# Optimization experiments

Measured on AMD Instinct MI355X. Metric: run time of the kernel, lower is better.

Reference implementation:

```python
import jax, jax.numpy as jnp
import numpy as np

B, S, K, N = 4, 2048, 4096, 4096

def setup_inputs() -> dict:
    key = jax.random.key(0)
    k1, k2, k3, k4 = jax.random.split(key, 4)
    # int8 quantized activations and weight (stored as int8, matmul accumulates int32)
    a = jax.random.randint(k1, (B, S, K), -128, 128, dtype=jnp.int32).astype(jnp.int8)
    w = jax.random.randint(k3, (K, N), -128, 128, dtype=jnp.int32).astype(jnp.int8)
    # dequant scales: per-token for activations, per-output-channel for weight
    a_s = (jax.random.uniform(k2, (B, S, 1), dtype=jnp.float32) + 0.5) * 0.01
    w_s = (jax.random.uniform(k4, (1, N), dtype=jnp.float32) + 0.5) * 0.01
    return {"a": a, "a_s": a_s, "w": w, "w_s": w_s}

def reference(a, a_s, w, w_s):
    # torch._int_mm loop with padding), fused with dequant epilogue.
    acc = jnp.einsum('bsk,kn->bsn', a, w, preferred_element_type=jnp.int32)
    # dequant: float32 accum * input_scale * weight_scale, cast to model dtype (fp16)
    out = (acc.astype(jnp.float32) * a_s * w_s).astype(jnp.float16)
    return out
```

## Files before the change

kernel.cpp:

```cpp
#include <hip/hip_runtime.h>
#include <cstdint>
#include <cstddef>


#define M_DIM 8192
#define N_DIM 4096
#define K_DIM 4096

#define PACKA_BLOCKS ((M_DIM * K_DIM / 4) / 256)
#define TRANS_BLOCKS ((N_DIM / 64) * (K_DIM / 64))

typedef int v4i  __attribute__((ext_vector_type(4)));
typedef int v16i __attribute__((ext_vector_type(16)));

__device__ __forceinline__ uint32_t pack4(int x, int y, int z, int w)
{
    return (uint32_t)(x & 0xff) | ((uint32_t)(y & 0xff) << 8) |
           ((uint32_t)(z & 0xff) << 16) | ((uint32_t)(w & 0xff) << 24);
}

__global__ void __launch_bounds__(256) prepare_kernel(
    const int* __restrict__ a, const int* __restrict__ w,
    uint8_t* __restrict__ pa, uint8_t* __restrict__ wt)
{
    __shared__ int lds[64][65];

    if (blockIdx.x < PACKA_BLOCKS) {
        const size_t idx = (size_t)blockIdx.x * 256 + threadIdx.x;
        int4 x = ((const int4*)a)[idx];
        ((uint32_t*)pa)[idx] = pack4(x.x, x.y, x.z, x.w);
        return;
    }

    const int tile = blockIdx.x - PACKA_BLOCKS;
    const int t  = threadIdx.x;
    const int n0 = (tile & 63) * 64;
    const int k0 = (tile >> 6) * 64;

#pragma unroll
    for (int i = 0; i < 4; ++i) {
        int v   = t + 256 * i;
        int row = v >> 4;
        int cq  = v & 15;
        int4 x = *(const int4*)(w + (size_t)(k0 + row) * N_DIM + n0 + cq * 4);
        lds[row][cq * 4 + 0] = x.x;
        lds[row][cq * 4 + 1] = x.y;
        lds[row][cq * 4 + 2] = x.z;
        lds[row][cq * 4 + 3] = x.w;
    }
    __syncthreads();

    const int n_local = t >> 2;
    const int c       = t & 3;
    uint32_t o[4];
#pragma unroll
    for (int j = 0; j < 4; ++j)
        o[j] = pack4(lds[c * 16 + j * 4 + 0][n_local],
                     lds[c * 16 + j * 4 + 1][n_local],
                     lds[c * 16 + j * 4 + 2][n_local],
                     lds[c * 16 + j * 4 + 3][n_local]);
    *(uint4*)(wt + (size_t)(n0 + n_local) * K_DIM + k0 + c * 16) =
        make_uint4(o[0], o[1], o[2], o[3]);
}

__device__ __forceinline__ void async_copy16(const void* gptr, void* lptr)
{
    __builtin_amdgcn_global_load_lds(
        (const __attribute__((address_space(1))) uint32_t*)gptr,
        (__attribute__((address_space(3))) uint32_t*)lptr,
        16, 0, 0);
}

#define VMCNT0() asm volatile("s_waitcnt vmcnt(0)" ::: "memory")

__global__ void __launch_bounds__(512, 2) int8_gemm_kernel(
    const uint8_t* __restrict__ A,
    const uint8_t* __restrict__ Wt,
    const float*   __restrict__ a_s,
    const float*   __restrict__ w_s,
    float*         __restrict__ out)
{
    __shared__ __align__(16) uint8_t sA[2][4][8][1024];
    __shared__ __align__(16) uint8_t sB[2][4][8][1024];

    const int tid   = threadIdx.x;
    const int wave  = tid >> 6;
    const int lane  = tid & 63;
    const int waveM = wave >> 2;
    const int waveN = wave & 3;

    const int bid = blockIdx.x;
    const int xc  = bid & 7;
    const int j   = bid >> 3;
    const int bm  = (xc & 3) * 8 + (j & 7);
    const int bn  = (xc >> 2) * 8 + (j >> 3);
    const int m0  = bm * 256;
    const int n0  = bn * 256;

    v16i acc[4][2];
#pragma unroll
    for (int i = 0; i < 4; ++i)
#pragma unroll
        for (int jj = 0; jj < 2; ++jj)
#pragma unroll
            for (int r = 0; r < 16; ++r)
                acc[i][jj][r] = 0;

    const uint8_t* aSrc = A  + (size_t)(m0 + wave * 32 + (lane & 31)) * K_DIM
                             + ((lane >> 5) << 4);
    const uint8_t* bSrc = Wt + (size_t)(n0 + wave * 32 + (lane & 31)) * K_DIM
                             + ((lane >> 5) << 4);

    auto stage_tile = [&](int buf, int kt) {
        const int ko = kt * 128;
#pragma unroll
        for (int s = 0; s < 4; ++s) {
            async_copy16(aSrc + ko + s * 32, &sA[buf][s][wave][0]);
            async_copy16(bSrc + ko + s * 32, &sB[buf][s][wave][0]);
        }
    };

    auto compute_kstep = [&](int buf, int s) {
        v4i af[4], bf[2];
#pragma unroll
        for (int mt = 0; mt < 4; ++mt)
            af[mt] = *(const v4i*)(&sA[buf][s][waveM * 4 + mt][lane * 16]);
#pragma unroll
        for (int nt = 0; nt < 2; ++nt)
            bf[nt] = *(const v4i*)(&sB[buf][s][waveN * 2 + nt][lane * 16]);
        __builtin_amdgcn_s_setprio(1);
#pragma unroll
        for (int mt = 0; mt < 4; ++mt)
#pragma unroll
            for (int nt = 0; nt < 2; ++nt)
                acc[mt][nt] = __builtin_amdgcn_mfma_i32_32x32x32_i8(
                    af[mt], bf[nt], acc[mt][nt], 0, 0, 0);
        __builtin_amdgcn_s_setprio(0);
    };

    const int NT = K_DIM / 128;

    stage_tile(0, 0);
    VMCNT0();
    __builtin_amdgcn_s_barrier();

    for (int kt = 0; kt < NT - 1; ++kt) {
        const int b = kt & 1;
        stage_tile(b ^ 1, kt + 1);
#pragma unroll
        for (int s = 0; s < 4; ++s)
            compute_kstep(b, s);
        VMCNT0();
        __builtin_amdgcn_s_barrier();
    }
#pragma unroll
    for (int s = 0; s < 4; ++s)
        compute_kstep((NT - 1) & 1, s);

    const int col   = lane & 31;
    const int rbase = (lane >> 5) * 4;

#pragma unroll
    for (int mt = 0; mt < 4; ++mt) {
        const int mrow0 = m0 + waveM * 128 + mt * 32 + rbase;
        float asv[16];
#pragma unroll
        for (int reg = 0; reg < 16; ++reg)
            asv[reg] = a_s[mrow0 + (reg & 3) + 8 * (reg >> 2)];
#pragma unroll
        for (int nt = 0; nt < 2; ++nt) {
            const int n = n0 + waveN * 64 + nt * 32 + col;
            const float wsv = w_s[n];
#pragma unroll
            for (int reg = 0; reg < 16; ++reg) {
                const int row = mrow0 + (reg & 3) + 8 * (reg >> 2);
                float v = (float)acc[mt][nt][reg] * asv[reg] * wsv;
                v = (float)(_Float16)v;
                out[(size_t)row * N_DIM + n] = v;
            }
        }
    }
}

extern "C" void kernel_launch(void* const* d_in, const int* in_sizes, int n_in,
                              void* d_out, int out_size, void* d_ws, size_t ws_size,
                              hipStream_t stream)
{
    const int*   a   = (const int*)  d_in[0];
    const float* a_s = (const float*)d_in[1];
    const int*   w   = (const int*)  d_in[2];
    const float* w_s = (const float*)d_in[3];
    float*       out = (float*)d_out;

    uint8_t* wt = (uint8_t*)d_ws;
    uint8_t* pa = (uint8_t*)d_ws + (size_t)N_DIM * K_DIM;

    prepare_kernel<<<PACKA_BLOCKS + TRANS_BLOCKS, 256, 0, stream>>>(a, w, pa, wt);

    int8_gemm_kernel<<<(M_DIM / 256) * (N_DIM / 256), 512, 0, stream>>>(
        pa, wt, a_s, w_s, out);
}
```

Before: 460.5 us.

## Pre-swizzle A and W into MFMA fragment layout and split-phase pipeline loads

```diff
diff --git a/kernel.cpp b/kernel.cpp
--- a/kernel.cpp
+++ b/kernel.cpp
@@ -7,8 +7,8 @@
 #define N_DIM 4096
 #define K_DIM 4096
 
-#define PACKA_BLOCKS ((M_DIM * K_DIM / 4) / 256)
-#define TRANS_BLOCKS ((N_DIM / 64) * (K_DIM / 64))
+#define PREP_A_BLOCKS ((M_DIM / 32) * (K_DIM / 128))
+#define PREP_W_BLOCKS ((N_DIM / 64) * (K_DIM / 64))
 
 typedef int v4i  __attribute__((ext_vector_type(4)));
 typedef int v16i __attribute__((ext_vector_type(16)));
@@ -21,19 +21,36 @@
 
 __global__ void __launch_bounds__(256) prepare_kernel(
     const int* __restrict__ a, const int* __restrict__ w,
-    uint8_t* __restrict__ pa, uint8_t* __restrict__ wt)
+    uint8_t* __restrict__ a_f, uint8_t* __restrict__ w_f)
 {
     __shared__ int lds[64][65];
-
-    if (blockIdx.x < PACKA_BLOCKS) {
-        const size_t idx = (size_t)blockIdx.x * 256 + threadIdx.x;
-        int4 x = ((const int4*)a)[idx];
-        ((uint32_t*)pa)[idx] = pack4(x.x, x.y, x.z, x.w);
+    const int t = threadIdx.x;
+
+    if (blockIdx.x < PREP_A_BLOCKS) {
+        uint32_t* l32 = (uint32_t*)&lds[0][0];
+        const int bm = blockIdx.x >> 5;
+        const int bk = blockIdx.x & 31;
+        const int m0 = bm * 32;
+        const int k0 = bk * 128;
+#pragma unroll
+        for (int i = 0; i < 4; ++i) {
+            const int f = i * 256 + t;
+            const int r = f >> 5;
+            const int c = (f << 2) & 127;
+            int4 x = *(const int4*)(a + (size_t)(m0 + r) * K_DIM + k0 + c);
+            uint32_t u = pack4(x.x, x.y, x.z, x.w);
+            const int region = c >> 5;
+            const int chunk  = r + (((c >> 4) & 1) << 5);
+            const int wd     = region * 256 + chunk * 4 + ((c & 15) >> 2);
+            l32[wd ^ ((region & 3) << 3)] = u;
+        }
+        __syncthreads();
+        uint4 o = ((const uint4*)l32)[t ^ (((t >> 6) & 3) << 1)];
+        *(uint4*)(a_f + ((size_t)bm * 128 + bk * 4) * 1024 + t * 16) = o;
         return;
     }
 
-    const int tile = blockIdx.x - PACKA_BLOCKS;
-    const int t  = threadIdx.x;
+    const int tile = blockIdx.x - PREP_A_BLOCKS;
     const int n0 = (tile & 63) * 64;
     const int k0 = (tile >> 6) * 64;
 
@@ -50,17 +67,22 @@
     }
     __syncthreads();
 
-    const int n_local = t >> 2;
-    const int c       = t & 3;
+    const int chunk  = t & 63;
+    const int r_out  = t >> 6;
+    const int nb     = r_out >> 1;
+    const int kk     = r_out & 1;
+    const int ncol   = nb * 32 + (chunk & 31);
+    const int parity = chunk >> 5;
+    const int rbase  = kk * 32 + parity * 16;
     uint32_t o[4];
 #pragma unroll
-    for (int j = 0; j < 4; ++j)
-        o[j] = pack4(lds[c * 16 + j * 4 + 0][n_local],
-                     lds[c * 16 + j * 4 + 1][n_local],
-                     lds[c * 16 + j * 4 + 2][n_local],
-                     lds[c * 16 + j * 4 + 3][n_local]);
-    *(uint4*)(wt + (size_t)(n0 + n_local) * K_DIM + k0 + c * 16) =
-        make_uint4(o[0], o[1], o[2], o[3]);
+    for (int q = 0; q < 4; ++q)
+        o[q] = pack4(lds[rbase + q * 4 + 0][ncol],
+                     lds[rbase + q * 4 + 1][ncol],
+                     lds[rbase + q * 4 + 2][ncol],
+                     lds[rbase + q * 4 + 3][ncol]);
+    *(uint4*)(w_f + (((size_t)(n0 >> 5) + nb) * 128 + (k0 >> 5) + kk) * 1024
+                  + chunk * 16) = make_uint4(o[0], o[1], o[2], o[3]);
 }
 
 __device__ __forceinline__ void async_copy16(const void* gptr, void* lptr)
@@ -71,11 +93,12 @@
         16, 0, 0);
 }
 
+#define VMCNT4() asm volatile("s_waitcnt vmcnt(4)" ::: "memory")
 #define VMCNT0() asm volatile("s_waitcnt vmcnt(0)" ::: "memory")
 
 __global__ void __launch_bounds__(512, 2) int8_gemm_kernel(
-    const uint8_t* __restrict__ A,
-    const uint8_t* __restrict__ Wt,
+    const uint8_t* __restrict__ Af,
+    const uint8_t* __restrict__ Wf,
     const float*   __restrict__ a_s,
     const float*   __restrict__ w_s,
     float*         __restrict__ out)
@@ -106,17 +129,14 @@
             for (int r = 0; r < 16; ++r)
                 acc[i][jj][r] = 0;
 
-    const uint8_t* aSrc = A  + (size_t)(m0 + wave * 32 + (lane & 31)) * K_DIM
-                             + ((lane >> 5) << 4);
-    const uint8_t* bSrc = Wt + (size_t)(n0 + wave * 32 + (lane & 31)) * K_DIM
-                             + ((lane >> 5) << 4);
-
-    auto stage_tile = [&](int buf, int kt) {
-        const int ko = kt * 128;
-#pragma unroll
-        for (int s = 0; s < 4; ++s) {
-            async_copy16(aSrc + ko + s * 32, &sA[buf][s][wave][0]);
-            async_copy16(bSrc + ko + s * 32, &sB[buf][s][wave][0]);
+    const uint8_t* aBase = Af + (((size_t)(m0 >> 5) + wave) * 128) * 1024 + lane * 16;
+    const uint8_t* bBase = Wf + (((size_t)(n0 >> 5) + wave) * 128) * 1024 + lane * 16;
+
+    auto stage2 = [&](int buf, int kt, int s0) {
+#pragma unroll
+        for (int s = s0; s < s0 + 2; ++s) {
+            async_copy16(aBase + (size_t)(kt * 4 + s) * 1024, &sA[buf][s][wave][0]);
+            async_copy16(bBase + (size_t)(kt * 4 + s) * 1024, &sB[buf][s][wave][0]);
         }
     };
 
@@ -140,22 +160,33 @@
 
     const int NT = K_DIM / 128;
 
-    stage_tile(0, 0);
-    VMCNT0();
+    stage2(0, 0, 0);
+    stage2(0, 0, 2);
+    VMCNT4();
     __builtin_amdgcn_s_barrier();
 
     for (int kt = 0; kt < NT - 1; ++kt) {
         const int b = kt & 1;
-        stage_tile(b ^ 1, kt + 1);
-#pragma unroll
-        for (int s = 0; s < 4; ++s)
-            compute_kstep(b, s);
+        stage2(b ^ 1, kt + 1, 0);
+        compute_kstep(b, 0);
+        compute_kstep(b, 1);
+        VMCNT4();
+        __builtin_amdgcn_s_barrier();
+        stage2(b ^ 1, kt + 1, 2);
+        compute_kstep(b, 2);
+        compute_kstep(b, 3);
+        VMCNT4();
+        __builtin_amdgcn_s_barrier();
+    }
+    {
+        const int b = (NT - 1) & 1;
+        compute_kstep(b, 0);
+        compute_kstep(b, 1);
         VMCNT0();
         __builtin_amdgcn_s_barrier();
-    }
-#pragma unroll
-    for (int s = 0; s < 4; ++s)
-        compute_kstep((NT - 1) & 1, s);
+        compute_kstep(b, 2);
+        compute_kstep(b, 3);
+    }
 
     const int col   = lane & 31;
     const int rbase = (lane >> 5) * 4;
@@ -192,11 +223,12 @@
     const float* w_s = (const float*)d_in[3];
     float*       out = (float*)d_out;
 
-    uint8_t* wt = (uint8_t*)d_ws;
-    uint8_t* pa = (uint8_t*)d_ws + (size_t)N_DIM * K_DIM;
-
-    prepare_kernel<<<PACKA_BLOCKS + TRANS_BLOCKS, 256, 0, stream>>>(a, w, pa, wt);
+    uint8_t* w_f = (uint8_t*)d_ws;
+    uint8_t* a_f = (uint8_t*)d_ws + (size_t)N_DIM * K_DIM;
+
+    prepare_kernel<<<PREP_A_BLOCKS + PREP_W_BLOCKS, 256, 0, stream>>>(
+        a, w, a_f, w_f);
 
     int8_gemm_kernel<<<(M_DIM / 256) * (N_DIM / 256), 512, 0, stream>>>(
-        pa, wt, a_s, w_s, out);
-}
+        a_f, w_f, a_s, w_s, out);
+}
```

Measured after the change: 406.0 us. 1.13x faster.
